# Performance work log

Hardware: AMD Instinct MI355X
Metric: run time of the kernel (lower is better)

Reference implementation:

```python
import jax, jax.numpy as jnp
import numpy as np

N = 100000
IN_DIM = 512
HID = (256, 256, 128)
NNZ = 3200000
SLOPE = 0.25  # leaky_relu negative slope


def _spmm(rows, cols, vals, X):
    # out[i] = sum_{e: rows[e]==i} vals[e] * X[cols[e]]  -> sparse [N,N] @ X
    return jax.ops.segment_sum(vals[:, None] * X[cols], rows, num_segments=N)


def setup_inputs() -> dict:
    key = jax.random.key(0)
    ks = jax.random.split(key, 10)
    x = jax.random.normal(ks[0], (N, IN_DIM), dtype=jnp.float32)
    adj_rows = jax.random.randint(ks[1], (NNZ,), 0, N, dtype=jnp.int32)
    adj_cols = jax.random.randint(ks[2], (NNZ,), 0, N, dtype=jnp.int32)
    adj_vals = jax.random.uniform(ks[3], (NNZ,), dtype=jnp.float32)
    # xavier_normal-ish init for weights, zeros for biases
    def xav(k, fan_in, fan_out):
        std = (2.0 / (fan_in + fan_out)) ** 0.5
        return std * jax.random.normal(k, (fan_in, fan_out), dtype=jnp.float32)
    W1 = xav(ks[4], IN_DIM, HID[0]); b1 = jnp.zeros((HID[0],), jnp.float32)
    W2 = xav(ks[5], HID[0], HID[1]); b2 = jnp.zeros((HID[1],), jnp.float32)
    W3 = xav(ks[6], HID[1], HID[2]); b3 = jnp.zeros((HID[2],), jnp.float32)
    return {"x": x, "adj_rows": adj_rows, "adj_cols": adj_cols, "adj_vals": adj_vals,
            "W1": W1, "b1": b1, "W2": W2, "b2": b2, "W3": W3, "b3": b3}


def reference(x, adj_rows, adj_cols, adj_vals, W1, b1, W2, b2, W3, b3):
    # Inference mode: F.dropout with training=False is identity.
    def layer(h, W, b):
        support = h @ W                       # dense GEMM [N, d_out]
        out = _spmm(adj_rows, adj_cols, adj_vals, support) + b
        return jax.nn.leaky_relu(out, SLOPE)
    h = layer(x, W1, b1)
    h = layer(h, W2, b2)
    h = layer(h, W3, b3)
    return h
```

## Files before the change

### kernel.cpp

```cpp
#include <hip/hip_runtime.h>

#define N_NODES 100000
#define NNZ_E   3200000
#define SLOPE   0.25f

#define NBUCK 782
#define PBLK  512
#define PCH   6250
#define CAP   6144

typedef __attribute__((ext_vector_type(8))) short bf16x8;
typedef __attribute__((ext_vector_type(4))) float f32x4;

__device__ __forceinline__ unsigned short f2b(float f) {
    union { float f; unsigned int u; } c; c.f = f;
    unsigned int u = c.u + 0x7fffu + ((c.u >> 16) & 1u);
    return (unsigned short)(u >> 16);
}
__device__ __forceinline__ unsigned int pack2(float a, float b) {
    return (unsigned int)f2b(a) | ((unsigned int)f2b(b) << 16);
}
__device__ __forceinline__ float b2f_lo(unsigned int u) {
    union { unsigned int u; float f; } c; c.u = u << 16; return c.f;
}
__device__ __forceinline__ float b2f_hi(unsigned int u) {
    union { unsigned int u; float f; } c; c.u = u & 0xffff0000u; return c.f;
}

__device__ __forceinline__ void load_lds16(const unsigned short* gp, unsigned short* lp) {
    __builtin_amdgcn_global_load_lds(
        (const __attribute__((address_space(1))) void*)gp,
        (__attribute__((address_space(3))) void*)lp, 16, 0, 0);
}

__global__ __launch_bounds__(256) void partition_kernel(
    const int* __restrict__ rows, const int* __restrict__ cols,
    const float* __restrict__ vals,
    int2* __restrict__ stagedRC, float* __restrict__ stagedV,
    int* __restrict__ offs , int* __restrict__ btot)
{
    __shared__ int hist[NBUCK];
    __shared__ int ts[256];
    const int blk = blockIdx.x, t = threadIdx.x;
    const int base = blk * PCH;

    for (int i = t; i < NBUCK; i += 256) hist[i] = 0;
    __syncthreads();
    for (int e = t; e < PCH; e += 256)
        atomicAdd(&hist[rows[base + e] >> 7], 1);
    __syncthreads();

    const int i0 = t << 2;
    int c0 = (i0 + 0 < NBUCK) ? hist[i0 + 0] : 0;
    int c1 = (i0 + 1 < NBUCK) ? hist[i0 + 1] : 0;
    int c2 = (i0 + 2 < NBUCK) ? hist[i0 + 2] : 0;
    int c3 = (i0 + 3 < NBUCK) ? hist[i0 + 3] : 0;
    int s = c0 + c1 + c2 + c3;
    ts[t] = s; __syncthreads();
    for (int off = 1; off < 256; off <<= 1) {
        int u = (t >= off) ? ts[t - off] : 0;
        __syncthreads();
        ts[t] += u;
        __syncthreads();
    }
    int ex = ts[t] - s;
    int o0 = ex, o1 = ex + c0, o2 = o1 + c1, o3 = o2 + c2;
    int* gof = offs + blk * (NBUCK + 1);
    if (i0 + 0 < NBUCK) { hist[i0 + 0] = o0; gof[i0 + 0] = o0; if (c0) atomicAdd(&btot[i0 + 0], c0); }
    if (i0 + 1 < NBUCK) { hist[i0 + 1] = o1; gof[i0 + 1] = o1; if (c1) atomicAdd(&btot[i0 + 1], c1); }
    if (i0 + 2 < NBUCK) { hist[i0 + 2] = o2; gof[i0 + 2] = o2; if (c2) atomicAdd(&btot[i0 + 2], c2); }
    if (i0 + 3 < NBUCK) { hist[i0 + 3] = o3; gof[i0 + 3] = o3; if (c3) atomicAdd(&btot[i0 + 3], c3); }
    if (t == 255) gof[NBUCK] = ts[255];
    __syncthreads();

    for (int e = t; e < PCH; e += 256) {
        int r = rows[base + e];
        int p = atomicAdd(&hist[r >> 7], 1);
        stagedRC[base + p] = make_int2(r, cols[base + e]);
        stagedV[base + p] = vals[base + e];
    }
}

__global__ __launch_bounds__(1024) void bscan_kernel(const int* __restrict__ btot,
                                                     int* __restrict__ bbase,
                                                     int* __restrict__ roff) {
    __shared__ int lds[1024];
    int t = threadIdx.x;
    int v = (t < NBUCK) ? btot[t] : 0;
    lds[t] = v; __syncthreads();
    for (int off = 1; off < 1024; off <<= 1) {
        int u = (t >= off) ? lds[t - off] : 0;
        __syncthreads();
        lds[t] += u;
        __syncthreads();
    }
    if (t < NBUCK) bbase[t] = lds[t] - v;
    if (t == 0) { bbase[NBUCK] = NNZ_E; roff[N_NODES] = NNZ_E; }
}

__global__ __launch_bounds__(256) void place_kernel(
    const int* __restrict__ offs, const int* __restrict__ bbase,
    const int2* __restrict__ stagedRC, const float* __restrict__ stagedV,
    int* __restrict__ roff, int2* __restrict__ epack)
{
    __shared__ int sstart[PBLK];
    __shared__ int spos[PBLK + 1];
    __shared__ int ts[256];
    __shared__ int eCol[CAP];
    __shared__ float eVal[CAP];
    __shared__ unsigned char eRow[CAP];
    __shared__ int cnt[128];
    __shared__ int rex[128];
    const int b = blockIdx.x, t = threadIdx.x;

    for (int i = t; i < PBLK; i += 256) {
        int s = offs[i * (NBUCK + 1) + b];
        int e = offs[i * (NBUCK + 1) + b + 1];
        sstart[i] = s;
        spos[i] = e - s;
    }
    __syncthreads();
    int l0 = spos[2 * t], l1 = spos[2 * t + 1];
    int s = l0 + l1;
    ts[t] = s; __syncthreads();
    for (int off = 1; off < 256; off <<= 1) {
        int u = (t >= off) ? ts[t - off] : 0;
        __syncthreads();
        ts[t] += u;
        __syncthreads();
    }
    int ex = ts[t] - s;
    spos[2 * t] = ex; spos[2 * t + 1] = ex + l0;
    if (t == 255) spos[PBLK] = ts[255];
    __syncthreads();
    int T = spos[PBLK];
    if (T > CAP) T = CAP;

    for (int x = t; x < T; x += 256) {
        int lo = 0, hi = PBLK;
        while (hi - lo > 1) { int mid = (lo + hi) >> 1; if (spos[mid] <= x) lo = mid; else hi = mid; }
        int g = lo * PCH + sstart[lo] + (x - spos[lo]);
        int2 rc = stagedRC[g];
        eRow[x] = (unsigned char)(rc.x & 127);
        eCol[x] = rc.y;
        eVal[x] = stagedV[g];
    }
    if (t < 128) cnt[t] = 0;
    __syncthreads();
    for (int x = t; x < T; x += 256) atomicAdd(&cnt[eRow[x]], 1);
    __syncthreads();
    int cv = (t < 128) ? cnt[t] : 0;
    if (t < 128) rex[t] = cv;
    __syncthreads();
    for (int off = 1; off < 128; off <<= 1) {
        int u = (t >= off && t < 128) ? rex[t - off] : 0;
        __syncthreads();
        if (t < 128) rex[t] += u;
        __syncthreads();
    }
    const int bb = bbase[b];
    int exl = 0;
    if (t < 128) exl = rex[t] - cv;
    __syncthreads();
    if (t < 128) {
        rex[t] = exl;
        cnt[t] = 0;
        int idx = (b << 7) + t;
        if (idx < N_NODES) roff[idx] = bb + exl;
    }
    __syncthreads();
    for (int x = t; x < T; x += 256) {
        int rl = eRow[x];
        int p = bb + rex[rl] + atomicAdd(&cnt[rl], 1);
        epack[p] = make_int2(eCol[x], __float_as_int(eVal[x]));
    }
}

__global__ __launch_bounds__(256) void wprep3_kernel(
    const float* __restrict__ W1, unsigned short* __restrict__ Wt1,
    const float* __restrict__ W2, unsigned short* __restrict__ Wt2,
    const float* __restrict__ W3, unsigned short* __restrict__ Wt3)
{
    int idx = blockIdx.x * blockDim.x + threadIdx.x;
    if (idx < 131072) {
        int n = idx >> 9, k = idx & 511;
        Wt1[idx] = f2b(W1[(size_t)k * 256 + n]);
    } else if (idx < 131072 + 65536) {
        int i = idx - 131072;
        int n = i >> 8, k = i & 255;
        Wt2[i] = f2b(W2[(size_t)k * 256 + n]);
    } else if (idx < 131072 + 65536 + 32768) {
        int i = idx - 131072 - 65536;
        int n = i >> 8, k = i & 255;
        Wt3[i] = f2b(W3[(size_t)k * 128 + n]);
    }
}

template<int AF32>
__global__ __launch_bounds__(256) void gemm256(
    const void* __restrict__ Av,
    const unsigned short* __restrict__ Bt,
    unsigned short* __restrict__ C,
    int M, int K)
{
    __shared__ __align__(16) unsigned short As[128 * 32];
    __shared__ __align__(16) unsigned short Bs[256 * 32];
    const int t = threadIdx.x;
    const int wave = t >> 6, lane = t & 63;
    const int wm = wave & 1, wn = wave >> 1;
    const int quad = lane >> 4, l16 = lane & 15;
    const int row0 = blockIdx.x * 128;

    f32x4 acc[4][8];
#pragma unroll
    for (int mt = 0; mt < 4; ++mt)
#pragma unroll
        for (int nt = 0; nt < 8; ++nt) acc[mt][nt] = (f32x4){0.f, 0.f, 0.f, 0.f};

    const int sr0 = wave * 16 + (lane >> 2);
    const int sc  = (lane & 3) << 3;

    const int arow = t >> 1, ahalf = t & 1;
    int araw = row0 + arow; if (araw > M - 1) araw = M - 1;
    const float* Af = (const float*)Av;
    const unsigned short* Ab = (const unsigned short*)Av;

    int ra0 = row0 + sr0;      if (ra0 > M - 1) ra0 = M - 1;
    int ra1 = row0 + sr0 + 64; if (ra1 > M - 1) ra1 = M - 1;

    for (int k0 = 0; k0 < K; k0 += 32) {
        __syncthreads();
        if (AF32) {
            const float* src = &Af[(size_t)araw * K + k0 + ahalf * 16];
            float4 f0 = *(const float4*)(src + 0);
            float4 f1 = *(const float4*)(src + 4);
            float4 f2 = *(const float4*)(src + 8);
            float4 f3 = *(const float4*)(src + 12);
            uint4 lo, hi;
            lo.x = pack2(f0.x, f0.y); lo.y = pack2(f0.z, f0.w);
            lo.z = pack2(f1.x, f1.y); lo.w = pack2(f1.z, f1.w);
            hi.x = pack2(f2.x, f2.y); hi.y = pack2(f2.z, f2.w);
            hi.z = pack2(f3.x, f3.y); hi.w = pack2(f3.z, f3.w);
            *(uint4*)&As[arow * 32 + ahalf * 16 + 0] = lo;
            *(uint4*)&As[arow * 32 + ahalf * 16 + 8] = hi;
        } else {
            load_lds16(&Ab[(size_t)ra0 * K + k0 + sc], &As[(size_t)wave * 512]);
            load_lds16(&Ab[(size_t)ra1 * K + k0 + sc], &As[(size_t)(wave + 4) * 512]);
        }
#pragma unroll
        for (int g = 0; g < 4; ++g)
            load_lds16(&Bt[(size_t)(g * 64 + sr0) * K + k0 + sc],
                       &Bs[(size_t)(g * 4 + wave) * 512]);
        __syncthreads();

        bf16x8 af[4], bf[8];
#pragma unroll
        for (int mt = 0; mt < 4; ++mt)
            af[mt] = *(const bf16x8*)&As[(wm * 64 + mt * 16 + l16) * 32 + quad * 8];
#pragma unroll
        for (int nt = 0; nt < 8; ++nt)
            bf[nt] = *(const bf16x8*)&Bs[(wn * 128 + nt * 16 + l16) * 32 + quad * 8];
#pragma unroll
        for (int mt = 0; mt < 4; ++mt)
#pragma unroll
            for (int nt = 0; nt < 8; ++nt)
                acc[mt][nt] = __builtin_amdgcn_mfma_f32_16x16x32_bf16(
                    af[mt], bf[nt], acc[mt][nt], 0, 0, 0);
    }

#pragma unroll
    for (int mt = 0; mt < 4; ++mt)
#pragma unroll
        for (int r = 0; r < 4; ++r) {
            int row = row0 + wm * 64 + mt * 16 + quad * 4 + r;
            if (row < M) {
#pragma unroll
                for (int nt = 0; nt < 8; ++nt) {
                    int col = wn * 128 + nt * 16 + l16;
                    C[(size_t)row * 256 + col] = f2b(acc[mt][nt][r]);
                }
            }
        }
}

__global__ __launch_bounds__(256) void gemm_bf16_128(
    const unsigned short* __restrict__ A,
    const unsigned short* __restrict__ Bt,
    unsigned short* __restrict__ C,
    int M, int K, int Nc)
{
    __shared__ __align__(16) unsigned short As[128 * 32];
    __shared__ __align__(16) unsigned short Bs[128 * 32];
    const int t = threadIdx.x;
    const int wave = t >> 6, lane = t & 63;
    const int wm = wave & 1, wn = wave >> 1;
    const int quad = lane >> 4, l16 = lane & 15;
    const int row0 = blockIdx.y * 128, col0 = blockIdx.x * 128;

    f32x4 acc[4][4];
#pragma unroll
    for (int mt = 0; mt < 4; ++mt)
#pragma unroll
        for (int nt = 0; nt < 4; ++nt) acc[mt][nt] = (f32x4){0.f, 0.f, 0.f, 0.f};

    const int sr0 = wave * 16 + (lane >> 2);
    const int sr1 = sr0 + 64;
    const int sc  = (lane & 3) << 3;

    int ra0 = row0 + sr0; if (ra0 > M - 1) ra0 = M - 1;
    int ra1 = row0 + sr1; if (ra1 > M - 1) ra1 = M - 1;
    const int rb0 = col0 + sr0;
    const int rb1 = col0 + sr1;

    for (int k0 = 0; k0 < K; k0 += 32) {
        __syncthreads();
        load_lds16(&A [(size_t)ra0 * K + k0 + sc], &As[(size_t)wave * 512]);
        load_lds16(&A [(size_t)ra1 * K + k0 + sc], &As[(size_t)(wave + 4) * 512]);
        load_lds16(&Bt[(size_t)rb0 * K + k0 + sc], &Bs[(size_t)wave * 512]);
        load_lds16(&Bt[(size_t)rb1 * K + k0 + sc], &Bs[(size_t)(wave + 4) * 512]);
        __syncthreads();

        bf16x8 af[4], bf[4];
#pragma unroll
        for (int mt = 0; mt < 4; ++mt)
            af[mt] = *(const bf16x8*)&As[(wm * 64 + mt * 16 + l16) * 32 + quad * 8];
#pragma unroll
        for (int nt = 0; nt < 4; ++nt)
            bf[nt] = *(const bf16x8*)&Bs[(wn * 64 + nt * 16 + l16) * 32 + quad * 8];
#pragma unroll
        for (int mt = 0; mt < 4; ++mt)
#pragma unroll
            for (int nt = 0; nt < 4; ++nt)
                acc[mt][nt] = __builtin_amdgcn_mfma_f32_16x16x32_bf16(
                    af[mt], bf[nt], acc[mt][nt], 0, 0, 0);
    }

#pragma unroll
    for (int mt = 0; mt < 4; ++mt)
#pragma unroll
        for (int r = 0; r < 4; ++r) {
            int row = row0 + wm * 64 + mt * 16 + quad * 4 + r;
            if (row < M) {
#pragma unroll
                for (int nt = 0; nt < 4; ++nt) {
                    int col = col0 + wn * 64 + nt * 16 + l16;
                    C[(size_t)row * Nc + col] = f2b(acc[mt][nt][r]);
                }
            }
        }
}

__global__ __launch_bounds__(256) void spmm256b_kernel(const int* __restrict__ row_off,
                                                       const int2* __restrict__ ep,
                                                       const unsigned short* __restrict__ sup,
                                                       const float* __restrict__ bias,
                                                       unsigned short* __restrict__ out) {
    int row = (blockIdx.x << 2) + (threadIdx.x >> 6);
    if (row >= N_NODES) return;
    const int lane = threadIdx.x & 63;
    const int s = row_off[row], e = row_off[row + 1];
    const int cb = lane << 2;
    float a0 = 0.f, a1 = 0.f, a2 = 0.f, a3 = 0.f;

    for (int base = s; base < e; base += 64) {
        const int idx = base + lane;
        int2 p = make_int2(0, 0);
        if (idx < e) p = ep[idx];
        const int rem = e - base;
        const int nb = (rem < 64) ? rem : 64;
        for (int jb = 0; jb < nb; jb += 8) {
#pragma unroll
            for (int j = 0; j < 8; ++j) {
                const int col = __builtin_amdgcn_readlane(p.x, jb + j);
                const float v = __int_as_float(__builtin_amdgcn_readlane(p.y, jb + j));
                const uint2 g = *(const uint2*)&sup[((size_t)col << 8) + cb];
                a0 += v * b2f_lo(g.x); a1 += v * b2f_hi(g.x);
                a2 += v * b2f_lo(g.y); a3 += v * b2f_hi(g.y);
            }
        }
    }
    float4 bv = *(const float4*)&bias[cb];
    a0 += bv.x; a1 += bv.y; a2 += bv.z; a3 += bv.w;
    a0 = (a0 >= 0.f) ? a0 : SLOPE * a0;
    a1 = (a1 >= 0.f) ? a1 : SLOPE * a1;
    a2 = (a2 >= 0.f) ? a2 : SLOPE * a2;
    a3 = (a3 >= 0.f) ? a3 : SLOPE * a3;
    ushort4 o; o.x = f2b(a0); o.y = f2b(a1); o.z = f2b(a2); o.w = f2b(a3);
    *(ushort4*)&out[((size_t)row << 8) + cb] = o;
}

__global__ __launch_bounds__(256) void spmm128f_kernel(const int* __restrict__ row_off,
                                                       const int2* __restrict__ ep,
                                                       const unsigned short* __restrict__ sup,
                                                       const float* __restrict__ bias,
                                                       float* __restrict__ out) {
    int row = (blockIdx.x << 2) + (threadIdx.x >> 6);
    if (row >= N_NODES) return;
    const int lane = threadIdx.x & 63;
    const int s = row_off[row], e = row_off[row + 1];
    const int cb = lane << 1;
    float a0 = 0.f, a1 = 0.f;

    for (int base = s; base < e; base += 64) {
        const int idx = base + lane;
        int2 p = make_int2(0, 0);
        if (idx < e) p = ep[idx];
        const int rem = e - base;
        const int nb = (rem < 64) ? rem : 64;
        for (int jb = 0; jb < nb; jb += 8) {
#pragma unroll
            for (int j = 0; j < 8; ++j) {
                const int col = __builtin_amdgcn_readlane(p.x, jb + j);
                const float v = __int_as_float(__builtin_amdgcn_readlane(p.y, jb + j));
                const unsigned int g = *(const unsigned int*)&sup[((size_t)col << 7) + cb];
                a0 += v * b2f_lo(g); a1 += v * b2f_hi(g);
            }
        }
    }
    float2 bv = *(const float2*)&bias[cb];
    a0 += bv.x; a1 += bv.y;
    a0 = (a0 >= 0.f) ? a0 : SLOPE * a0;
    a1 = (a1 >= 0.f) ? a1 : SLOPE * a1;
    *(float2*)&out[((size_t)row << 7) + cb] = make_float2(a0, a1);
}

extern "C" void kernel_launch(void* const* d_in, const int* in_sizes, int n_in,
                              void* d_out, int out_size, void* d_ws, size_t ws_size,
                              hipStream_t stream) {
    const float* x     = (const float*)d_in[0];
    const int*   arows = (const int*)d_in[1];
    const int*   acols = (const int*)d_in[2];
    const float* avals = (const float*)d_in[3];
    const float* W1 = (const float*)d_in[4];
    const float* b1 = (const float*)d_in[5];
    const float* W2 = (const float*)d_in[6];
    const float* b2 = (const float*)d_in[7];
    const float* W3 = (const float*)d_in[8];
    const float* b3 = (const float*)d_in[9];
    float* out = (float*)d_out;

    char* ws = (char*)d_ws;
    int2*  stagedRC = (int2*) (ws);
    float* stagedV  = (float*)(ws + 25600000);
    int*   offs     = (int*)  (ws + 38400000);
    int*   btot     = (int*)  (ws + 40003584);
    int*   bbase    = (int*)  (ws + 40006720);
    unsigned short* bufS = (unsigned short*)(ws + 102400000);
    unsigned short* bufH = (unsigned short*)(ws + 153600000);
    int2*  epack = (int2*)(ws + 204800000);
    int*   roff  = (int*) (ws + 230400000);
    unsigned short* Wt1 = (unsigned short*)(ws + 230800016);
    unsigned short* Wt2 = (unsigned short*)(ws + 231062160);
    unsigned short* Wt3 = (unsigned short*)(ws + 231193232);

    hipMemsetAsync(btot, 0, NBUCK * sizeof(int), stream);
    partition_kernel<<<PBLK, 256, 0, stream>>>(arows, acols, avals, stagedRC, stagedV, offs, btot);
    bscan_kernel<<<1, 1024, 0, stream>>>(btot, bbase, roff);
    place_kernel<<<NBUCK, 256, 0, stream>>>(offs, bbase, stagedRC, stagedV, roff, epack);

    wprep3_kernel<<<896, 256, 0, stream>>>(W1, Wt1, W2, Wt2, W3, Wt3);

    const int gyc = (N_NODES + 127) / 128;

    gemm256<1><<<gyc, 256, 0, stream>>>(x, Wt1, bufS, N_NODES, 512);
    spmm256b_kernel<<<25000, 256, 0, stream>>>(roff, epack, bufS, b1, bufH);
    gemm256<0><<<gyc, 256, 0, stream>>>(bufH, Wt2, bufS, N_NODES, 256);
    spmm256b_kernel<<<25000, 256, 0, stream>>>(roff, epack, bufS, b2, bufH);
    gemm_bf16_128<<<dim3(1, gyc), 256, 0, stream>>>(bufH, Wt3, bufS, N_NODES, 256, 128);
    spmm128f_kernel<<<25000, 256, 0, stream>>>(roff, epack, bufS, b3, out);
}
```

Baseline: 1.206 ms.

## Double-buffer GEMM LDS tiles and pack staged edges into single int2

The bf16 GEMM now double-buffers its A and B LDS tiles. The next k-step's global loads are issued before the MFMAs on the current tile, which cuts the syncs per step to one. The CSR build packs the local row, column and value into a single int2 staging record. place_kernel now walks each source chunk's segment serially per thread, dropping the LDS edge cache, prefix scan and binary search. The serial per-segment loops (each about 8 edges long) and the two passes over global staging memory may cost more than the removed LDS staging.

```diff
diff --git a/kernel.cpp b/kernel.cpp
--- a/kernel.cpp
+++ b/kernel.cpp
@@ -7,7 +7,6 @@
 #define NBUCK 782
 #define PBLK  512
 #define PCH   6250
-#define CAP   6144
 
 typedef __attribute__((ext_vector_type(8))) short bf16x8;
 typedef __attribute__((ext_vector_type(4))) float f32x4;
@@ -36,7 +35,7 @@
 __global__ __launch_bounds__(256) void partition_kernel(
     const int* __restrict__ rows, const int* __restrict__ cols,
     const float* __restrict__ vals,
-    int2* __restrict__ stagedRC, float* __restrict__ stagedV,
+    int2* __restrict__ stagedP,
     int* __restrict__ offs , int* __restrict__ btot)
 {
     __shared__ int hist[NBUCK];
@@ -76,8 +75,8 @@
     for (int e = t; e < PCH; e += 256) {
         int r = rows[base + e];
         int p = atomicAdd(&hist[r >> 7], 1);
-        stagedRC[base + p] = make_int2(r, cols[base + e]);
-        stagedV[base + p] = vals[base + e];
+        stagedP[base + p] = make_int2(((r & 127) << 17) | cols[base + e],
+                                      __float_as_int(vals[base + e]));
     }
 }
 
@@ -100,15 +99,11 @@
 
 __global__ __launch_bounds__(256) void place_kernel(
     const int* __restrict__ offs, const int* __restrict__ bbase,
-    const int2* __restrict__ stagedRC, const float* __restrict__ stagedV,
+    const int2* __restrict__ stagedP,
     int* __restrict__ roff, int2* __restrict__ epack)
 {
     __shared__ int sstart[PBLK];
-    __shared__ int spos[PBLK + 1];
-    __shared__ int ts[256];
-    __shared__ int eCol[CAP];
-    __shared__ float eVal[CAP];
-    __shared__ unsigned char eRow[CAP];
+    __shared__ int slen[PBLK];
     __shared__ int cnt[128];
     __shared__ int rex[128];
     const int b = blockIdx.x, t = threadIdx.x;
@@ -117,38 +112,21 @@
         int s = offs[i * (NBUCK + 1) + b];
         int e = offs[i * (NBUCK + 1) + b + 1];
         sstart[i] = s;
-        spos[i] = e - s;
-    }
-    __syncthreads();
-    int l0 = spos[2 * t], l1 = spos[2 * t + 1];
-    int s = l0 + l1;
-    ts[t] = s; __syncthreads();
-    for (int off = 1; off < 256; off <<= 1) {
-        int u = (t >= off) ? ts[t - off] : 0;
-        __syncthreads();
-        ts[t] += u;
-        __syncthreads();
-    }
-    int ex = ts[t] - s;
-    spos[2 * t] = ex; spos[2 * t + 1] = ex + l0;
-    if (t == 255) spos[PBLK] = ts[255];
-    __syncthreads();
-    int T = spos[PBLK];
-    if (T > CAP) T = CAP;
-
-    for (int x = t; x < T; x += 256) {
-        int lo = 0, hi = PBLK;
-        while (hi - lo > 1) { int mid = (lo + hi) >> 1; if (spos[mid] <= x) lo = mid; else hi = mid; }
-        int g = lo * PCH + sstart[lo] + (x - spos[lo]);
-        int2 rc = stagedRC[g];
-        eRow[x] = (unsigned char)(rc.x & 127);
-        eCol[x] = rc.y;
-        eVal[x] = stagedV[g];
+        slen[i] = e - s;
     }
     if (t < 128) cnt[t] = 0;
     __syncthreads();
-    for (int x = t; x < T; x += 256) atomicAdd(&cnt[eRow[x]], 1);
-    __syncthreads();
+
+    for (int i = t; i < PBLK; i += 256) {
+        const int s0 = sstart[i], len = slen[i];
+        const int* p = (const int*)(stagedP + (size_t)i * PCH + s0);
+        for (int j = 0; j < len; ++j) {
+            int rl = (p[2 * j] >> 17) & 127;
+            atomicAdd(&cnt[rl], 1);
+        }
+    }
+    __syncthreads();
+
     int cv = (t < 128) ? cnt[t] : 0;
     if (t < 128) rex[t] = cv;
     __syncthreads();
@@ -159,8 +137,7 @@
         __syncthreads();
     }
     const int bb = bbase[b];
-    int exl = 0;
-    if (t < 128) exl = rex[t] - cv;
+    int exl = (t < 128) ? (rex[t] - cv) : 0;
     __syncthreads();
     if (t < 128) {
         rex[t] = exl;
@@ -169,10 +146,16 @@
         if (idx < N_NODES) roff[idx] = bb + exl;
     }
     __syncthreads();
-    for (int x = t; x < T; x += 256) {
-        int rl = eRow[x];
-        int p = bb + rex[rl] + atomicAdd(&cnt[rl], 1);
-        epack[p] = make_int2(eCol[x], __float_as_int(eVal[x]));
+
+    for (int i = t; i < PBLK; i += 256) {
+        const int s0 = sstart[i], len = slen[i];
+        const int2* p = stagedP + (size_t)i * PCH + s0;
+        for (int j = 0; j < len; ++j) {
+            int2 ed = p[j];
+            int rl = (ed.x >> 17) & 127;
+            int pos = bb + rex[rl] + atomicAdd(&cnt[rl], 1);
+            epack[pos] = make_int2(ed.x & 0x1FFFF, ed.y);
+        }
     }
 }
 
@@ -203,8 +186,8 @@
     unsigned short* __restrict__ C,
     int M, int K)
 {
-    __shared__ __align__(16) unsigned short As[128 * 32];
-    __shared__ __align__(16) unsigned short Bs[256 * 32];
+    __shared__ __align__(16) unsigned short As[2][128 * 32];
+    __shared__ __align__(16) unsigned short Bs[2][256 * 32];
     const int t = threadIdx.x;
     const int wave = t >> 6, lane = t & 63;
     const int wm = wave & 1, wn = wave >> 1;
@@ -228,44 +211,77 @@
     int ra0 = row0 + sr0;      if (ra0 > M - 1) ra0 = M - 1;
     int ra1 = row0 + sr0 + 64; if (ra1 > M - 1) ra1 = M - 1;
 
-    for (int k0 = 0; k0 < K; k0 += 32) {
-        __syncthreads();
-        if (AF32) {
-            const float* src = &Af[(size_t)araw * K + k0 + ahalf * 16];
-            float4 f0 = *(const float4*)(src + 0);
-            float4 f1 = *(const float4*)(src + 4);
-            float4 f2 = *(const float4*)(src + 8);
-            float4 f3 = *(const float4*)(src + 12);
+    const int nsteps = K >> 5;
+
+    if (AF32) {
+        const float* src = &Af[(size_t)araw * K + ahalf * 16];
+        float4 f0 = *(const float4*)(src + 0);
+        float4 f1 = *(const float4*)(src + 4);
+        float4 f2 = *(const float4*)(src + 8);
+        float4 f3 = *(const float4*)(src + 12);
+        uint4 lo, hi;
+        lo.x = pack2(f0.x, f0.y); lo.y = pack2(f0.z, f0.w);
+        lo.z = pack2(f1.x, f1.y); lo.w = pack2(f1.z, f1.w);
+        hi.x = pack2(f2.x, f2.y); hi.y = pack2(f2.z, f2.w);
+        hi.z = pack2(f3.x, f3.y); hi.w = pack2(f3.z, f3.w);
+        *(uint4*)&As[0][arow * 32 + ahalf * 16 + 0] = lo;
+        *(uint4*)&As[0][arow * 32 + ahalf * 16 + 8] = hi;
+    } else {
+        load_lds16(&Ab[(size_t)ra0 * K + sc], &As[0][wave * 512]);
+        load_lds16(&Ab[(size_t)ra1 * K + sc], &As[0][(wave + 4) * 512]);
+    }
+#pragma unroll
+    for (int g = 0; g < 4; ++g)
+        load_lds16(&Bt[(size_t)(g * 64 + sr0) * K + sc], &Bs[0][(g * 4 + wave) * 512]);
+    __syncthreads();
+
+    for (int it = 0; it < nsteps; ++it) {
+        const int cur = it & 1, nxt = cur ^ 1;
+        const int k1 = (it + 1) << 5;
+        const bool pf = (it + 1 < nsteps);
+        float4 f0, f1, f2, f3;
+
+        if (pf) {
+            if (AF32) {
+                const float* src = &Af[(size_t)araw * K + k1 + ahalf * 16];
+                f0 = *(const float4*)(src + 0);
+                f1 = *(const float4*)(src + 4);
+                f2 = *(const float4*)(src + 8);
+                f3 = *(const float4*)(src + 12);
+            } else {
+                load_lds16(&Ab[(size_t)ra0 * K + k1 + sc], &As[nxt][wave * 512]);
+                load_lds16(&Ab[(size_t)ra1 * K + k1 + sc], &As[nxt][(wave + 4) * 512]);
+            }
+#pragma unroll
+            for (int g = 0; g < 4; ++g)
+                load_lds16(&Bt[(size_t)(g * 64 + sr0) * K + k1 + sc],
+                           &Bs[nxt][(g * 4 + wave) * 512]);
+        }
+
+        bf16x8 af[4], bf[8];
+#pragma unroll
+        for (int mt = 0; mt < 4; ++mt)
+            af[mt] = *(const bf16x8*)&As[cur][(wm * 64 + mt * 16 + l16) * 32 + quad * 8];
+#pragma unroll
+        for (int nt = 0; nt < 8; ++nt)
+            bf[nt] = *(const bf16x8*)&Bs[cur][(wn * 128 + nt * 16 + l16) * 32 + quad * 8];
+#pragma unroll
+        for (int mt = 0; mt < 4; ++mt)
+#pragma unroll
+            for (int nt = 0; nt < 8; ++nt)
+                acc[mt][nt] = __builtin_amdgcn_mfma_f32_16x16x32_bf16(
+                    af[mt], bf[nt], acc[mt][nt], 0, 0, 0);
+
+        if (pf && AF32) {
             uint4 lo, hi;
             lo.x = pack2(f0.x, f0.y); lo.y = pack2(f0.z, f0.w);
             lo.z = pack2(f1.x, f1.y); lo.w = pack2(f1.z, f1.w);
             hi.x = pack2(f2.x, f2.y); hi.y = pack2(f2.z, f2.w);
             hi.z = pack2(f3.x, f3.y); hi.w = pack2(f3.z, f3.w);
-            *(uint4*)&As[arow * 32 + ahalf * 16 + 0] = lo;
-            *(uint4*)&As[arow * 32 + ahalf * 16 + 8] = hi;
-        } else {
-            load_lds16(&Ab[(size_t)ra0 * K + k0 + sc], &As[(size_t)wave * 512]);
-            load_lds16(&Ab[(size_t)ra1 * K + k0 + sc], &As[(size_t)(wave + 4) * 512]);
-        }
-#pragma unroll
-        for (int g = 0; g < 4; ++g)
-            load_lds16(&Bt[(size_t)(g * 64 + sr0) * K + k0 + sc],
-                       &Bs[(size_t)(g * 4 + wave) * 512]);
-        __syncthreads();
-
-        bf16x8 af[4], bf[8];
-#pragma unroll
-        for (int mt = 0; mt < 4; ++mt)
-            af[mt] = *(const bf16x8*)&As[(wm * 64 + mt * 16 + l16) * 32 + quad * 8];
-#pragma unroll
-        for (int nt = 0; nt < 8; ++nt)
-            bf[nt] = *(const bf16x8*)&Bs[(wn * 128 + nt * 16 + l16) * 32 + quad * 8];
-#pragma unroll
-        for (int mt = 0; mt < 4; ++mt)
-#pragma unroll
-            for (int nt = 0; nt < 8; ++nt)
-                acc[mt][nt] = __builtin_amdgcn_mfma_f32_16x16x32_bf16(
-                    af[mt], bf[nt], acc[mt][nt], 0, 0, 0);
+            *(uint4*)&As[nxt][arow * 32 + ahalf * 16 + 0] = lo;
+            *(uint4*)&As[nxt][arow * 32 + ahalf * 16 + 8] = hi;
+        }
+        __syncthreads();
     }
 
 #pragma unroll
@@ -440,11 +456,10 @@
     float* out = (float*)d_out;
 
     char* ws = (char*)d_ws;
-    int2*  stagedRC = (int2*) (ws);
-    float* stagedV  = (float*)(ws + 25600000);
-    int*   offs     = (int*)  (ws + 38400000);
-    int*   btot     = (int*)  (ws + 40003584);
-    int*   bbase    = (int*)  (ws + 40006720);
+    int2*  stagedP = (int2*)(ws);
+    int*   offs    = (int*) (ws + 25600000);
+    int*   btot    = (int*) (ws + 27203584);
+    int*   bbase   = (int*) (ws + 27207168);
     unsigned short* bufS = (unsigned short*)(ws + 102400000);
     unsigned short* bufH = (unsigned short*)(ws + 153600000);
     int2*  epack = (int2*)(ws + 204800000);
@@ -454,9 +469,9 @@
     unsigned short* Wt3 = (unsigned short*)(ws + 231193232);
 
     hipMemsetAsync(btot, 0, NBUCK * sizeof(int), stream);
-    partition_kernel<<<PBLK, 256, 0, stream>>>(arows, acols, avals, stagedRC, stagedV, offs, btot);
+    partition_kernel<<<PBLK, 256, 0, stream>>>(arows, acols, avals, stagedP, offs, btot);
     bscan_kernel<<<1, 1024, 0, stream>>>(btot, bbase, roff);
-    place_kernel<<<NBUCK, 256, 0, stream>>>(offs, bbase, stagedRC, stagedV, roff, epack);
+    place_kernel<<<NBUCK, 256, 0, stream>>>(offs, bbase, stagedP, roff, epack);
 
     wprep3_kernel<<<896, 256, 0, stream>>>(W1, Wt1, W2, Wt2, W3, Wt3);
 
```

Measured after the change: 1.155 ms. 4.2% less time.
